# Performance work log

Hardware: AMD Instinct MI355X
Metric: run time of the kernel (lower is better)

Reference implementation:

```python
import jax, jax.numpy as jnp
import numpy as np

B, L, D, HD = 8, 4096, 1024, 16
H = D // HD


def setup_inputs() -> dict:
    key = jax.random.key(0)
    ks = jax.random.split(key, 16)
    s = 0.02
    return {
        "x": jax.random.normal(ks[0], (B, L, D), dtype=jnp.float32),
        "gamma": jnp.ones((D,), jnp.float32),
        "beta": jnp.zeros((D,), jnp.float32),
        "qw": jax.random.normal(ks[1], (D, D), jnp.float32) * s,
        "qb": jnp.zeros((D,), jnp.float32),
        "kw": jax.random.normal(ks[2], (D, D), jnp.float32) * s,
        "kb": jnp.zeros((D,), jnp.float32),
        "vw": jax.random.normal(ks[3], (D, D), jnp.float32) * s,
        "vb": jnp.zeros((D,), jnp.float32),
        "ow": jax.random.normal(ks[4], (D, D), jnp.float32) * s,
        "ob": jnp.zeros((D,), jnp.float32),
        "iw": jax.random.normal(ks[5], (H, D), jnp.float32) * s,
        "ib": jnp.zeros((H,), jnp.float32),
        "fw": jax.random.normal(ks[6], (H, D), jnp.float32) * s,
        "fb": jnp.zeros((H,), jnp.float32),
    }


def _layernorm(x, gamma, beta, eps=1e-5):
    mu = jnp.mean(x, axis=-1, keepdims=True)
    var = jnp.mean(jnp.square(x - mu), axis=-1, keepdims=True)
    return (x - mu) * jax.lax.rsqrt(var + eps) * gamma + beta


def _forward(x, gamma, beta, qw, qb, kw, kb, vw, vb, ow, ob, iw, ib, fw, fb):
    b, l, d = x.shape
    h_, dh = H, HD
    xn = _layernorm(x, gamma, beta)                    # [B,L,D]
    # Projections vectorized over time (the per-step norm/proj is time-independent)
    q = (xn @ qw.T + qb).reshape(b, l, h_, dh)
    k = ((xn @ kw.T + kb) / np.sqrt(dh)).reshape(b, l, h_, dh)
    v = (xn @ vw.T + vb).reshape(b, l, h_, dh)
    i_t = xn @ iw.T + ib                               # [B,L,H]
    f_t = xn @ fw.T + fb                               # [B,L,H]

    def step(carry, inp):
        C, n, m = carry
        qt, kt, vt, it, ft = inp                       # [B,H,Dh]x3, [B,H]x2
        m_new = jnp.maximum(ft + m, it)
        f = jnp.exp(ft + m - m_new)                    # [B,H]
        i = jnp.exp(it - m_new)                        # [B,H]
        vk = jnp.einsum('bhd,bhe->bhde', vt, kt)
        C_new = f[..., None, None] * C + i[..., None, None] * vk
        n_new = f[..., None] * n + i[..., None] * kt
        Cq = jnp.einsum('bhde,bhd->bhe', C_new, qt)
        denom = jnp.maximum(jnp.abs(jnp.sum(n_new * qt, axis=-1, keepdims=True)), 1.0)
        ht = (Cq / denom).reshape(b, d)
        return (C_new, n_new, m_new), ht

    init = (jnp.zeros((b, h_, dh, dh), x.dtype),
            jnp.zeros((b, h_, dh), x.dtype),
            jnp.zeros((b, h_), x.dtype))
    xs = (jnp.swapaxes(q, 0, 1), jnp.swapaxes(k, 0, 1), jnp.swapaxes(v, 0, 1),
          jnp.swapaxes(i_t, 0, 1), jnp.swapaxes(f_t, 0, 1))
    _, hs = jax.lax.scan(step, init, xs)               # [L,B,D]
    hs = jnp.swapaxes(hs, 0, 1)                        # [B,L,D]
    out = hs @ ow.T + ob
    return x + out                                     # dropout is identity in eval


def reference(x, gamma, beta, qw, qb, kw, kb, vw, vb, ow, ob, iw, ib, fw, fb):
    return _forward(x, gamma, beta, qw, qb, kw, kb, vw, vb, ow, ob, iw, ib, fw, fb)
```

## Files before the change

kernel.cpp:

```cpp
#include <hip/hip_runtime.h>
#include <stdint.h>

#define Bq 8
#define Lq 4096
#define Dq 1024
#define Hq 64
#define Mq (Bq*Lq)
#define CH 64
#define NC (Lq/CH)
#define TC (Bq*Hq*NC)
#define RECF 288

typedef short bf16x8 __attribute__((ext_vector_type(8)));
typedef float f32x4  __attribute__((ext_vector_type(4)));

__device__ __forceinline__ float b2f(unsigned short u) {
  union { unsigned int i; float f; } v; v.i = ((unsigned int)u) << 16; return v.f;
}
__device__ __forceinline__ unsigned short f2b(float f) {
  union { float f; unsigned int i; } v; v.f = f;
  unsigned int r = v.i + 0x7fffu + ((v.i >> 16) & 1u);
  return (unsigned short)(r >> 16);
}
__device__ __forceinline__ bf16x8 pack8(float4 a, float4 b) {
  bf16x8 r;
  r[0] = (short)f2b(a.x); r[1] = (short)f2b(a.y); r[2] = (short)f2b(a.z); r[3] = (short)f2b(a.w);
  r[4] = (short)f2b(b.x); r[5] = (short)f2b(b.y); r[6] = (short)f2b(b.z); r[7] = (short)f2b(b.w);
  return r;
}

__device__ __forceinline__ void gload_lds16(const unsigned short* g, unsigned short* l) {
  __builtin_amdgcn_global_load_lds(
      (const __attribute__((address_space(1))) unsigned int*)g,
      (__attribute__((address_space(3))) unsigned int*)l, 16, 0, 0);
}

__global__ void classify_kernel(const unsigned short* __restrict__ w, unsigned int* flag) {
  __shared__ unsigned int s_nz, s_ib;
  if (threadIdx.x == 0) { s_nz = 0; s_ib = 0; }
  __syncthreads();
  unsigned int nz = 0, ib = 0;
  for (int i = threadIdx.x; i < 8192; i += 256) {
    unsigned short u = w[2 * i];
    if (u) {
      nz++;
      unsigned int e = (u >> 7) & 0xFFu;
      if (e >= 0x31u && e <= 0x9Du) ib++;
    }
  }
  atomicAdd(&s_nz, nz); atomicAdd(&s_ib, ib);
  __syncthreads();
  if (threadIdx.x == 0) *flag = (s_nz > 0 && 4u * s_ib >= 3u * s_nz) ? 1u : 0u;
}

__global__ void sentinel_kernel(unsigned short* out, int n) {
  int i = blockIdx.x * 256 + threadIdx.x;
  if (i < n) out[i] = 0x447A;
}

__global__ void wconv_kernel(const void* __restrict__ wv, unsigned short* __restrict__ o,
                             const unsigned int* __restrict__ flagp) {
  const int isbf = (int)*flagp;
  const size_t i = ((size_t)blockIdx.x * 256 + threadIdx.x) * 8;
  if (isbf) {
    *(bf16x8*)(o + i) = *(const bf16x8*)((const unsigned short*)wv + i);
  } else {
    const float* wf = (const float*)wv;
    float4 a = *(const float4*)(wf + i);
    float4 b = *(const float4*)(wf + i + 4);
    *(bf16x8*)(o + i) = pack8(a, b);
  }
}

__global__ void ln_kernel(const void* __restrict__ xv,
                          const void* __restrict__ gv,
                          const void* __restrict__ bev,
                          unsigned short* __restrict__ xn,
                          const unsigned int* __restrict__ flagp) {
  const int isbf = (int)*flagp;
  const int row = blockIdx.x;
  const int t = threadIdx.x;
  const size_t base = (size_t)row * Dq;
  float v0, v1, v2, v3, g0, g1, g2, g3, e0, e1, e2, e3;
  if (isbf) {
    ushort4 u  = *(const ushort4*)((const unsigned short*)xv + base + t * 4);
    ushort4 g  = *(const ushort4*)((const unsigned short*)gv + t * 4);
    ushort4 be = *(const ushort4*)((const unsigned short*)bev + t * 4);
    v0 = b2f(u.x); v1 = b2f(u.y); v2 = b2f(u.z); v3 = b2f(u.w);
    g0 = b2f(g.x); g1 = b2f(g.y); g2 = b2f(g.z); g3 = b2f(g.w);
    e0 = b2f(be.x); e1 = b2f(be.y); e2 = b2f(be.z); e3 = b2f(be.w);
  } else {
    float4 u  = *(const float4*)((const float*)xv + base + t * 4);
    float4 g  = *(const float4*)((const float*)gv + t * 4);
    float4 be = *(const float4*)((const float*)bev + t * 4);
    v0 = u.x; v1 = u.y; v2 = u.z; v3 = u.w;
    g0 = g.x; g1 = g.y; g2 = g.z; g3 = g.w;
    e0 = be.x; e1 = be.y; e2 = be.z; e3 = be.w;
  }
  float s  = v0 + v1 + v2 + v3;
  float ss = v0*v0 + v1*v1 + v2*v2 + v3*v3;
#pragma unroll
  for (int off = 32; off >= 1; off >>= 1) {
    s  += __shfl_xor(s,  off, 64);
    ss += __shfl_xor(ss, off, 64);
  }
  __shared__ float sb[8];
  const int w = t >> 6, lane = t & 63;
  if (lane == 0) { sb[w] = s; sb[4 + w] = ss; }
  __syncthreads();
  s  = sb[0] + sb[1] + sb[2] + sb[3];
  ss = sb[4] + sb[5] + sb[6] + sb[7];
  const float mu   = s * (1.0f / Dq);
  const float var  = ss * (1.0f / Dq) - mu * mu;
  const float rstd = rsqrtf(var + 1e-5f);
  ushort4 o;
  o.x = f2b((v0 - mu) * rstd * g0 + e0);
  o.y = f2b((v1 - mu) * rstd * g1 + e1);
  o.z = f2b((v2 - mu) * rstd * g2 + e2);
  o.w = f2b((v3 - mu) * rstd * g3 + e3);
  *(ushort4*)(xn + base + t * 4) = o;
}

__device__ __forceinline__ void gemm_epilogue(
    f32x4 acc[4][4], int row0, int col0, int wm, int wn, int lane,
    const void* biasv, const void* residv, void* out,
    int N, float scale, int out_mode, int out_layout, int isbf) {
  const int colL = lane & 15;
  const int rq   = lane >> 4;
  const int wf32 = (out_mode == 1) || (out_mode == 2 && !isbf);
#pragma unroll
  for (int nt = 0; nt < 4; ++nt) {
    const int col = col0 + wn * 64 + nt * 16 + colL;
    if (col >= N) continue;
    const float bv = isbf ? b2f(((const unsigned short*)biasv)[col])
                          : ((const float*)biasv)[col];
#pragma unroll
    for (int mt = 0; mt < 4; ++mt) {
      const int rowb = row0 + wm * 64 + mt * 16 + rq * 4;
#pragma unroll
      for (int r = 0; r < 4; ++r) {
        const int row = rowb + r;
        size_t idx;
        if (out_layout == 1) {
          const int bb2 = row >> 12, t = row & 4095;
          idx = ((((size_t)bb2 * Hq + (col >> 4)) << 12) + t) * 16 + (col & 15);
        } else if (out_layout == 2) {
          const int bb2 = row >> 12, t = row & 4095;
          idx = (((size_t)bb2 * Hq + col) << 12) + t;
        } else {
          idx = (size_t)row * N + col;
        }
        float val = (acc[mt][nt][r] + bv) * scale;
        if (residv) {
          const size_t ridx = (size_t)row * N + col;
          val += isbf ? b2f(((const unsigned short*)residv)[ridx])
                      : ((const float*)residv)[ridx];
        }
        if (wf32) ((float*)out)[idx] = val;
        else ((unsigned short*)out)[idx] = f2b(val);
      }
    }
  }
}

__global__ void gemm_bt(const unsigned short* __restrict__ A,
                        const void* __restrict__ Wv,
                        const void* __restrict__ biasv,
                        const void* __restrict__ residv,
                        void* __restrict__ out,
                        int N, int K, float scale, int out_mode, int out_layout,
                        const unsigned int* __restrict__ flagp) {
  __shared__ unsigned short smA[128 * 32];
  __shared__ unsigned short smB[128 * 32];
  const int isbf = (int)*flagp;
  const int tid  = threadIdx.x;
  const int w    = tid >> 6;
  const int lane = tid & 63;
  const int wm   = w >> 1;
  const int wn   = w & 1;
  const int row0 = blockIdx.x * 128;
  const int col0 = blockIdx.y * 128;

  const int c0 = tid, c1 = tid + 256;
  const int ar0 = row0 + (c0 >> 2), ak0 = (c0 & 3) * 8;
  const int ar1 = row0 + (c1 >> 2), ak1 = (c1 & 3) * 8;
  int br0 = col0 + (c0 >> 2), bk0 = (c0 & 3) * 8;
  int br1 = col0 + (c1 >> 2), bk1 = (c1 & 3) * 8;
  if (br0 >= N) br0 = N - 1;
  if (br1 >= N) br1 = N - 1;
  const size_t aro0 = (size_t)ar0 * K + ak0;
  const size_t aro1 = (size_t)ar1 * K + ak1;
  const size_t bro0 = (size_t)br0 * K + bk0;
  const size_t bro1 = (size_t)br1 * K + bk1;

  f32x4 acc[4][4];
#pragma unroll
  for (int i = 0; i < 4; ++i)
#pragma unroll
    for (int j = 0; j < 4; ++j) acc[i][j] = (f32x4){0.f, 0.f, 0.f, 0.f};

  const int mrow = lane & 15;
  const int kq8  = (lane >> 4) * 8;

  for (int k0 = 0; k0 < K; k0 += 32) {
    bf16x8 ta0 = *(const bf16x8*)(A + aro0 + k0);
    bf16x8 ta1 = *(const bf16x8*)(A + aro1 + k0);
    bf16x8 tb0, tb1;
    if (isbf) {
      const unsigned short* W = (const unsigned short*)Wv;
      tb0 = *(const bf16x8*)(W + bro0 + k0);
      tb1 = *(const bf16x8*)(W + bro1 + k0);
    } else {
      const float* W = (const float*)Wv;
      float4 w00 = *(const float4*)(W + bro0 + k0);
      float4 w01 = *(const float4*)(W + bro0 + k0 + 4);
      float4 w10 = *(const float4*)(W + bro1 + k0);
      float4 w11 = *(const float4*)(W + bro1 + k0 + 4);
      tb0 = pack8(w00, w01);
      tb1 = pack8(w10, w11);
    }
    __syncthreads();
    *(bf16x8*)(smA + c0 * 8) = ta0;
    *(bf16x8*)(smA + c1 * 8) = ta1;
    *(bf16x8*)(smB + c0 * 8) = tb0;
    *(bf16x8*)(smB + c1 * 8) = tb1;
    __syncthreads();
    bf16x8 a[4], bb[4];
#pragma unroll
    for (int mt = 0; mt < 4; ++mt)
      a[mt] = *(const bf16x8*)(smA + (wm * 64 + mt * 16 + mrow) * 32 + kq8);
#pragma unroll
    for (int nt = 0; nt < 4; ++nt)
      bb[nt] = *(const bf16x8*)(smB + (wn * 64 + nt * 16 + mrow) * 32 + kq8);
#pragma unroll
    for (int mt = 0; mt < 4; ++mt)
#pragma unroll
      for (int nt = 0; nt < 4; ++nt)
        acc[mt][nt] = __builtin_amdgcn_mfma_f32_16x16x32_bf16(a[mt], bb[nt], acc[mt][nt], 0, 0, 0);
  }
  gemm_epilogue(acc, row0, col0, wm, wn, lane, biasv, residv, out,
                N, scale, out_mode, out_layout, isbf);
}

__global__ void __launch_bounds__(256)
gemm16(const unsigned short* __restrict__ A,
       const unsigned short* __restrict__ W,
       const void* __restrict__ biasv,
       const void* __restrict__ residv,
       void* __restrict__ out,
       float scale, int out_mode, int out_layout,
       const unsigned int* __restrict__ flagp) {
  __shared__ unsigned short smA[128 * 32];
  __shared__ unsigned short smB[128 * 32];
  const int isbf = (int)*flagp;
  const int tid  = threadIdx.x;
  const int w    = tid >> 6;
  const int lane = tid & 63;
  const int wm   = w >> 1;
  const int wn   = w & 1;
  const int row0 = blockIdx.x * 128;
  const int col0 = blockIdx.y * 128;

  const int rA0 = (w * 2) * 16 + (lane >> 2);
  const size_t aoff0 = (size_t)(row0 + rA0) * Dq + (lane & 3) * 8;
  const size_t aoff1 = aoff0 + (size_t)16 * Dq;
  const size_t boff0 = (size_t)(col0 + rA0) * Dq + (lane & 3) * 8;
  const size_t boff1 = boff0 + (size_t)16 * Dq;
  unsigned short* ldsA0 = smA + w * 1024;
  unsigned short* ldsA1 = smA + w * 1024 + 512;
  unsigned short* ldsB0 = smB + w * 1024;
  unsigned short* ldsB1 = smB + w * 1024 + 512;

  f32x4 acc[4][4];
#pragma unroll
  for (int i = 0; i < 4; ++i)
#pragma unroll
    for (int j = 0; j < 4; ++j) acc[i][j] = (f32x4){0.f, 0.f, 0.f, 0.f};

  const int mrow = lane & 15;
  const int kq8  = (lane >> 4) * 8;

  for (int k0 = 0; k0 < Dq; k0 += 32) {
    __syncthreads();
    gload_lds16(A + aoff0 + k0, ldsA0);
    gload_lds16(A + aoff1 + k0, ldsA1);
    gload_lds16(W + boff0 + k0, ldsB0);
    gload_lds16(W + boff1 + k0, ldsB1);
    __syncthreads();
    bf16x8 a[4], bb[4];
#pragma unroll
    for (int mt = 0; mt < 4; ++mt)
      a[mt] = *(const bf16x8*)(smA + (wm * 64 + mt * 16 + mrow) * 32 + kq8);
#pragma unroll
    for (int nt = 0; nt < 4; ++nt)
      bb[nt] = *(const bf16x8*)(smB + (wn * 64 + nt * 16 + mrow) * 32 + kq8);
#pragma unroll
    for (int mt = 0; mt < 4; ++mt)
#pragma unroll
      for (int nt = 0; nt < 4; ++nt)
        acc[mt][nt] = __builtin_amdgcn_mfma_f32_16x16x32_bf16(a[mt], bb[nt], acc[mt][nt], 0, 0, 0);
  }
  gemm_epilogue(acc, row0, col0, wm, wn, lane, biasv, residv, out,
                Dq, scale, out_mode, out_layout, isbf);
}

__device__ __forceinline__ void deposit16(float* __restrict__ dstrow, int xw,
                                          bf16x8 lo, bf16x8 hi) {
  float t[16];
#pragma unroll
  for (int j = 0; j < 8; ++j) t[j] = b2f((unsigned short)lo[j]);
#pragma unroll
  for (int j = 0; j < 8; ++j) t[8 + j] = b2f((unsigned short)hi[j]);
#pragma unroll
  for (int qd = 0; qd < 4; ++qd) {
    *(float4*)(dstrow + ((qd << 2) ^ xw)) =
        make_float4(t[qd * 4], t[qd * 4 + 1], t[qd * 4 + 2], t[qd * 4 + 3]);
  }
}


__global__ void __launch_bounds__(64, 1)
summary_kernel(const unsigned short* __restrict__ k,
               const unsigned short* __restrict__ v,
               const float* __restrict__ itg,
               const float* __restrict__ ftg,
               float* __restrict__ sum) {
  __shared__ float sk[CH * 16], sv[CH * 16], sp[CH];
  const int bid = blockIdx.x;
  const int bh  = bid >> 6;
  const int c   = bid & 63;
  const int lane = threadIdx.x;
  const int e  = lane & 15;
  const int dg = lane >> 4;
  const int d0 = dg * 4;
  const size_t qkvb = ((size_t)bh * Lq + (size_t)c * CH) * 16;
  const size_t gb   = (size_t)bh * Lq + (size_t)c * CH;

  float fv = ftg[gb + lane];
  float iv = itg[gb + lane];
  float F = fv;
#pragma unroll
  for (int off = 1; off < 64; off <<= 1) {
    float tt = __shfl_up(F, off, 64);
    if (lane >= off) F += tt;
  }
  float wv = iv - F;
  float Ml = wv;
#pragma unroll
  for (int off = 1; off < 64; off <<= 1)
    Ml = fmaxf(Ml, __shfl_xor(Ml, off, 64));
  const float Ftot = __shfl(F, 63, 64);

  const int xw = ((lane >> 1) & 3) << 2;
  {
    const unsigned short* kp = k + qkvb + (size_t)lane * 16;
    const unsigned short* vp = v + qkvb + (size_t)lane * 16;
    bf16x8 a0 = *(const bf16x8*)kp, a1 = *(const bf16x8*)(kp + 8);
    bf16x8 b0 = *(const bf16x8*)vp, b1 = *(const bf16x8*)(vp + 8);
    deposit16(sk + lane * 16, xw, a0, a1);
    deposit16(sv + lane * 16, xw, b0, b1);
    sp[lane] = __expf(wv - Ml);
  }
  float C0 = 0, C1 = 0, C2 = 0, C3 = 0;
  float g0 = 0, g1 = 0, g2 = 0, g3 = 0;
#pragma unroll 4
  for (int s = 0; s < CH; ++s) {
    const int x = ((s >> 1) & 3) << 2;
    const float* kr = sk + s * 16;
    const float* vr = sv + s * 16;
    const float p  = sp[s];
    const float ke = kr[e ^ x];
    const float4 kq = *(const float4*)(kr + (d0 ^ x));
    const float4 vq = *(const float4*)(vr + (d0 ^ x));
    const float a = p * ke;
    C0 = fmaf(a, vq.x, C0); C1 = fmaf(a, vq.y, C1);
    C2 = fmaf(a, vq.z, C2); C3 = fmaf(a, vq.w, C3);
    g0 = fmaf(p, kq.x, g0); g1 = fmaf(p, kq.y, g1);
    g2 = fmaf(p, kq.z, g2); g3 = fmaf(p, kq.w, g3);
  }
  float* rec = sum + (size_t)bid * RECF;
  *(float4*)(rec + e * 16 + d0) = make_float4(C0, C1, C2, C3);
  if (e == 0) *(float4*)(rec + 256 + d0) = make_float4(g0, g1, g2, g3);
  if (lane == 0) { rec[272] = Ml; rec[273] = Ftot; }
}

__global__ void __launch_bounds__(64, 1)
combine_kernel(float* __restrict__ sum) {
  const int bh = blockIdx.x;
  const int lane = threadIdx.x;
  float* base = sum + (size_t)bh * NC * RECF;
  float4 Sc = make_float4(0.f, 0.f, 0.f, 0.f);
  float Sn = 0.f;
  float m = 0.f;
  float4 G = *(float4*)(base + lane * 4);
  float gn = (lane < 16) ? base[256 + lane] : 0.f;
  float Ml = base[272], F = base[273];
  for (int c = 0; c < NC; ++c) {
    float* rec = base + (size_t)c * RECF;
    float4 Gn = make_float4(0.f, 0.f, 0.f, 0.f);
    float gnn = 0.f, Mln = 0.f, Fn = 0.f;
    if (c + 1 < NC) {
      float* rn = rec + RECF;
      Gn = *(float4*)(rn + lane * 4);
      if (lane < 16) gnn = rn[256 + lane];
      Mln = rn[272]; Fn = rn[273];
    }
    *(float4*)(rec + lane * 4) = Sc;
    if (lane < 16) rec[256 + lane] = Sn;
    if (lane == 0) rec[272] = m;
    const float mx = fmaxf(m, Ml);
    const float al = __expf(m - mx);
    const float be = __expf(Ml - mx);
    Sc.x = fmaf(al, Sc.x, be * G.x);
    Sc.y = fmaf(al, Sc.y, be * G.y);
    Sc.z = fmaf(al, Sc.z, be * G.z);
    Sc.w = fmaf(al, Sc.w, be * G.w);
    Sn = fmaf(al, Sn, be * gn);
    m = F + mx;
    G = Gn; gn = gnn; Ml = Mln; F = Fn;
  }
}

__global__ void __launch_bounds__(64, 1)
chunk_scan_kernel(const unsigned short* __restrict__ q,
                  const unsigned short* __restrict__ k,
                  const unsigned short* __restrict__ v,
                  const float* __restrict__ itg,
                  const float* __restrict__ ftg,
                  const float* __restrict__ sum,
                  unsigned short* __restrict__ hout) {
  __shared__ float sk[CH * 16], sq[CH * 16], sv[CH * 16], sg[2 * CH];
  const int bid = blockIdx.x;
  const int bh  = bid >> 6;
  const int c   = bid & 63;
  const int b   = bh >> 6;
  const int h   = bh & 63;
  const int lane = threadIdx.x;
  const int e  = lane & 15;
  const int dg = lane >> 4;
  const int d0 = dg * 4;
  const size_t qkvb = ((size_t)bh * Lq + (size_t)c * CH) * 16;
  const size_t gb   = (size_t)bh * Lq + (size_t)c * CH;
  const size_t ob   = (size_t)b * Lq * Dq + (size_t)h * 16 + (size_t)c * CH * Dq;

  const float* rec = sum + (size_t)bid * RECF;
  const float4 Cv = *(const float4*)(rec + e * 16 + d0);
  const float4 nv = *(const float4*)(rec + 256 + d0);
  float m = rec[272];
  float C0 = Cv.x, C1 = Cv.y, C2 = Cv.z, C3 = Cv.w;
  float n0 = nv.x, n1 = nv.y, n2 = nv.z, n3 = nv.w;

  const int xw = ((lane >> 1) & 3) << 2;
  {
    const unsigned short* kp = k + qkvb + (size_t)lane * 16;
    const unsigned short* qp = q + qkvb + (size_t)lane * 16;
    const unsigned short* vp = v + qkvb + (size_t)lane * 16;
    bf16x8 a0 = *(const bf16x8*)kp, a1 = *(const bf16x8*)(kp + 8);
    bf16x8 b0 = *(const bf16x8*)qp, b1 = *(const bf16x8*)(qp + 8);
    bf16x8 c0v = *(const bf16x8*)vp, c1v = *(const bf16x8*)(vp + 8);
    deposit16(sk + lane * 16, xw, a0, a1);
    deposit16(sq + lane * 16, xw, b0, b1);
    deposit16(sv + lane * 16, xw, c0v, c1v);
    sg[lane] = itg[gb + lane];
    sg[CH + lane] = ftg[gb + lane];
  }

#pragma unroll 4
  for (int s = 0; s < CH; ++s) {
    const int x = ((s >> 1) & 3) << 2;
    const float* kr = sk + s * 16;
    const float* qr = sq + s * 16;
    const float* vr = sv + s * 16;
    const float itc = sg[s];
    const float ftc = sg[CH + s];
    const float ke  = kr[e ^ x];
    const float4 kq4 = *(const float4*)(kr + (d0 ^ x));
    const float4 qq4 = *(const float4*)(qr + (d0 ^ x));
    const float4 vq4 = *(const float4*)(vr + (d0 ^ x));
    const float fm = ftc + m;
    const float mn = fmaxf(fm, itc);
    const float fg = __expf(fm - mn);
    const float ig = __expf(itc - mn);
    m = mn;
    const float a = ig * ke;
    C0 = fmaf(fg, C0, a * vq4.x);
    C1 = fmaf(fg, C1, a * vq4.y);
    C2 = fmaf(fg, C2, a * vq4.z);
    C3 = fmaf(fg, C3, a * vq4.w);
    n0 = fmaf(fg, n0, ig * kq4.x);
    n1 = fmaf(fg, n1, ig * kq4.y);
    n2 = fmaf(fg, n2, ig * kq4.z);
    n3 = fmaf(fg, n3, ig * kq4.w);
    float cq = fmaf(C3, qq4.w, fmaf(C2, qq4.z, fmaf(C1, qq4.y, C0 * qq4.x)));
    float dn = fmaf(n3, qq4.w, fmaf(n2, qq4.z, fmaf(n1, qq4.y, n0 * qq4.x)));
    cq += __shfl_xor(cq, 16, 64);
    cq += __shfl_xor(cq, 32, 64);
    dn += __shfl_xor(dn, 16, 64);
    dn += __shfl_xor(dn, 32, 64);
    const float denom = fmaxf(fabsf(dn), 1.0f);
    if (dg == 0) hout[ob + (size_t)s * Dq + e] = f2b(cq / denom);
  }
}

__global__ void __launch_bounds__(64, 1)
scan_kernel(const unsigned short* __restrict__ q,
            const unsigned short* __restrict__ k,
            const unsigned short* __restrict__ v,
            const float* __restrict__ itg,
            const float* __restrict__ ftg,
            unsigned short* __restrict__ hout) {
  __shared__ float sk[CH * 16], sq[CH * 16], sv[CH * 16], sg[2 * CH];
  const int bh = blockIdx.x;
  const int b  = bh >> 6;
  const int h  = bh & 63;
  const int lane = threadIdx.x;
  const int e  = lane & 15;
  const int dg = lane >> 4;
  const int d0 = dg * 4;
  const size_t qkvb = (size_t)bh * Lq * 16;
  const size_t gb   = (size_t)bh * Lq;
  const size_t ob   = (size_t)b * Lq * Dq + (size_t)h * 16;

  float C0 = 0, C1 = 0, C2 = 0, C3 = 0;
  float n0 = 0, n1 = 0, n2 = 0, n3 = 0;
  float m = 0.f;

  bf16x8 rk0, rk1, rq0, rq1, rv0, rv1;
  float rit, rft;
  {
    const unsigned short* kp = k + qkvb + (size_t)lane * 16;
    const unsigned short* qp = q + qkvb + (size_t)lane * 16;
    const unsigned short* vp = v + qkvb + (size_t)lane * 16;
    rk0 = *(const bf16x8*)kp; rk1 = *(const bf16x8*)(kp + 8);
    rq0 = *(const bf16x8*)qp; rq1 = *(const bf16x8*)(qp + 8);
    rv0 = *(const bf16x8*)vp; rv1 = *(const bf16x8*)(vp + 8);
    rit = itg[gb + lane]; rft = ftg[gb + lane];
  }

  const int xw = ((lane >> 1) & 3) << 2;
  const int NT = Lq / CH;
  for (int c = 0; c < NT; ++c) {
    deposit16(sk + lane * 16, xw, rk0, rk1);
    deposit16(sq + lane * 16, xw, rq0, rq1);
    deposit16(sv + lane * 16, xw, rv0, rv1);
    sg[lane] = rit; sg[CH + lane] = rft;
    if (c + 1 < NT) {
      const size_t off = qkvb + ((size_t)(c + 1) * CH + lane) * 16;
      const unsigned short* kp = k + off;
      const unsigned short* qp = q + off;
      const unsigned short* vp = v + off;
      rk0 = *(const bf16x8*)kp; rk1 = *(const bf16x8*)(kp + 8);
      rq0 = *(const bf16x8*)qp; rq1 = *(const bf16x8*)(qp + 8);
      rv0 = *(const bf16x8*)vp; rv1 = *(const bf16x8*)(vp + 8);
      rit = itg[gb + (size_t)(c + 1) * CH + lane];
      rft = ftg[gb + (size_t)(c + 1) * CH + lane];
    }
#pragma unroll 4
    for (int s = 0; s < CH; ++s) {
      const int x = ((s >> 1) & 3) << 2;
      const float* kr = sk + s * 16;
      const float* qr = sq + s * 16;
      const float* vr = sv + s * 16;
      const float itc = sg[s];
      const float ftc = sg[CH + s];
      const float ke  = kr[e ^ x];
      const float4 kq4 = *(const float4*)(kr + (d0 ^ x));
      const float4 qq4 = *(const float4*)(qr + (d0 ^ x));
      const float4 vq4 = *(const float4*)(vr + (d0 ^ x));
      const float fm = ftc + m;
      const float mn = fmaxf(fm, itc);
      const float fg = __expf(fm - mn);
      const float ig = __expf(itc - mn);
      m = mn;
      const float a = ig * ke;
      C0 = fmaf(fg, C0, a * vq4.x);
      C1 = fmaf(fg, C1, a * vq4.y);
      C2 = fmaf(fg, C2, a * vq4.z);
      C3 = fmaf(fg, C3, a * vq4.w);
      n0 = fmaf(fg, n0, ig * kq4.x);
      n1 = fmaf(fg, n1, ig * kq4.y);
      n2 = fmaf(fg, n2, ig * kq4.z);
      n3 = fmaf(fg, n3, ig * kq4.w);
      float cq = fmaf(C3, qq4.w, fmaf(C2, qq4.z, fmaf(C1, qq4.y, C0 * qq4.x)));
      float dn = fmaf(n3, qq4.w, fmaf(n2, qq4.z, fmaf(n1, qq4.y, n0 * qq4.x)));
      cq += __shfl_xor(cq, 16, 64);
      cq += __shfl_xor(cq, 32, 64);
      dn += __shfl_xor(dn, 16, 64);
      dn += __shfl_xor(dn, 32, 64);
      const float denom = fmaxf(fabsf(dn), 1.0f);
      if (dg == 0) hout[ob + (size_t)(c * CH + s) * Dq + e] = f2b(cq / denom);
    }
  }
}

extern "C" void kernel_launch(void* const* d_in, const int* in_sizes, int n_in,
                              void* d_out, int out_size, void* d_ws, size_t ws_size,
                              hipStream_t stream) {
  const void* x     = d_in[0];
  const void* gamma = d_in[1];
  const void* beta  = d_in[2];
  const void* qw    = d_in[3];
  const void* qbv   = d_in[4];
  const void* kw    = d_in[5];
  const void* kbv   = d_in[6];
  const void* vw    = d_in[7];
  const void* vbv   = d_in[8];
  const void* ow    = d_in[9];
  const void* obv   = d_in[10];
  const void* iw    = d_in[11];
  const void* ibv   = d_in[12];
  const void* fw    = d_in[13];
  const void* fbv   = d_in[14];

  const size_t bufBytes  = (size_t)Mq * Dq * 2;
  const size_t gateBytes = (size_t)Mq * Hq * 4;
  const size_t sumBytes  = (size_t)TC * RECF * 4;
  const size_t wBytes    = (size_t)Dq * Dq * 2;
  const size_t need_old   = 4 * bufBytes + 2 * gateBytes + 4096;
  const size_t need_chunk = need_old + sumBytes;
  const size_t need_fast  = need_chunk + 4 * wBytes;
  if (ws_size < need_old) {
    sentinel_kernel<<<(out_size + 255) / 256, 256, 0, stream>>>((unsigned short*)d_out, out_size);
    return;
  }
  const int chunked = (ws_size >= need_chunk);
  const int fast    = (ws_size >= need_fast);

  char* ws = (char*)d_ws;
  unsigned short* xnb = (unsigned short*)ws; ws += bufBytes;
  unsigned short* qbf = (unsigned short*)ws; ws += bufBytes;
  unsigned short* kbf = (unsigned short*)ws; ws += bufBytes;
  unsigned short* vbf = (unsigned short*)ws; ws += bufBytes;
  float* itb = (float*)ws; ws += gateBytes;
  float* ftb = (float*)ws; ws += gateBytes;
  unsigned int* flagp = (unsigned int*)ws; ws += 4096;
  float* sumb = (float*)ws; ws += sumBytes;
  unsigned short* wqb = (unsigned short*)ws; ws += wBytes;
  unsigned short* wkb = (unsigned short*)ws; ws += wBytes;
  unsigned short* wvb = (unsigned short*)ws; ws += wBytes;
  unsigned short* wob = (unsigned short*)ws; ws += wBytes;
  unsigned short* hbf = xnb;

  classify_kernel<<<1, 256, 0, stream>>>((const unsigned short*)qw, flagp);
  ln_kernel<<<Mq, 256, 0, stream>>>(x, gamma, beta, xnb, flagp);
  if (fast) {
    const int wgrid = (Dq * Dq / 8) / 256;
    wconv_kernel<<<wgrid, 256, 0, stream>>>(qw, wqb, flagp);
    wconv_kernel<<<wgrid, 256, 0, stream>>>(kw, wkb, flagp);
    wconv_kernel<<<wgrid, 256, 0, stream>>>(vw, wvb, flagp);
    wconv_kernel<<<wgrid, 256, 0, stream>>>(ow, wob, flagp);
    gemm16<<<dim3(Mq / 128, Dq / 128), 256, 0, stream>>>(xnb, wqb, qbv, nullptr, qbf, 1.0f,  0, 1, flagp);
    gemm16<<<dim3(Mq / 128, Dq / 128), 256, 0, stream>>>(xnb, wkb, kbv, nullptr, kbf, 0.25f, 0, 1, flagp);
    gemm16<<<dim3(Mq / 128, Dq / 128), 256, 0, stream>>>(xnb, wvb, vbv, nullptr, vbf, 1.0f,  0, 1, flagp);
  } else {
    gemm_bt<<<dim3(Mq / 128, 8), 256, 0, stream>>>(xnb, qw, qbv, nullptr, qbf, Dq, Dq, 1.0f,  0, 1, flagp);
    gemm_bt<<<dim3(Mq / 128, 8), 256, 0, stream>>>(xnb, kw, kbv, nullptr, kbf, Dq, Dq, 0.25f, 0, 1, flagp);
    gemm_bt<<<dim3(Mq / 128, 8), 256, 0, stream>>>(xnb, vw, vbv, nullptr, vbf, Dq, Dq, 1.0f,  0, 1, flagp);
  }
  gemm_bt<<<dim3(Mq / 128, 1), 256, 0, stream>>>(xnb, iw, ibv, nullptr, itb, Hq, Dq, 1.0f,  1, 2, flagp);
  gemm_bt<<<dim3(Mq / 128, 1), 256, 0, stream>>>(xnb, fw, fbv, nullptr, ftb, Hq, Dq, 1.0f,  1, 2, flagp);
  if (chunked) {
    summary_kernel<<<TC, 64, 0, stream>>>(kbf, vbf, itb, ftb, sumb);
    combine_kernel<<<Bq * Hq, 64, 0, stream>>>(sumb);
    chunk_scan_kernel<<<TC, 64, 0, stream>>>(qbf, kbf, vbf, itb, ftb, sumb, hbf);
  } else {
    scan_kernel<<<Bq * Hq, 64, 0, stream>>>(qbf, kbf, vbf, itb, ftb, hbf);
  }
  if (fast) {
    gemm16<<<dim3(Mq / 128, Dq / 128), 256, 0, stream>>>(hbf, wob, obv, x, d_out, 1.0f, 2, 0, flagp);
  } else {
    gemm_bt<<<dim3(Mq / 128, 8), 256, 0, stream>>>(hbf, ow, obv, x, d_out, Dq, Dq, 1.0f, 2, 0, flagp);
  }
}
```

Before: 1.215 ms.

## Remap GEMM tiles per XCD and compute chunk summaries with split-bf16 MFMA

The GEMM grid becomes one-dimensional, and block indices are remapped so that each of the 8 XCDs handles a contiguous band of 32 row tiles across all 8 column tiles. This is meant to improve L2 reuse of the A rows within each XCD. Separately, the chunk summary kernel now keeps k and v as bf16 in shared memory and computes the 16x16 C outer-product sum with MFMA 16x16x32 bf16 instructions. The p*v operand is split into hi and lo bf16 parts to preserve accuracy, which adds conversion work and a small precision risk in exchange for fewer scalar FMAs.

```diff
diff --git a/kernel.cpp b/kernel.cpp
--- a/kernel.cpp
+++ b/kernel.cpp
@@ -258,8 +258,13 @@
   const int lane = tid & 63;
   const int wm   = w >> 1;
   const int wn   = w & 1;
-  const int row0 = blockIdx.x * 128;
-  const int col0 = blockIdx.y * 128;
+  const int o    = blockIdx.x;
+  const int xcd  = o & 7;
+  const int slot = o >> 3;
+  const int rloc = slot >> 3;
+  const int cloc = slot & 7;
+  const int row0 = (xcd * 32 + rloc) * 128;
+  const int col0 = cloc * 128;
 
   const int rA0 = (w * 2) * 16 + (lane >> 2);
   const size_t aoff0 = (size_t)(row0 + rA0) * Dq + (lane & 3) * 8;
@@ -325,14 +330,13 @@
                const float* __restrict__ itg,
                const float* __restrict__ ftg,
                float* __restrict__ sum) {
-  __shared__ float sk[CH * 16], sv[CH * 16], sp[CH];
+  __shared__ unsigned short skb[CH * 16];
+  __shared__ unsigned short svb[CH * 16];
+  __shared__ float sp[CH];
   const int bid = blockIdx.x;
   const int bh  = bid >> 6;
   const int c   = bid & 63;
   const int lane = threadIdx.x;
-  const int e  = lane & 15;
-  const int dg = lane >> 4;
-  const int d0 = dg * 4;
   const size_t qkvb = ((size_t)bh * Lq + (size_t)c * CH) * 16;
   const size_t gb   = (size_t)bh * Lq + (size_t)c * CH;
 
@@ -351,36 +355,48 @@
     Ml = fmaxf(Ml, __shfl_xor(Ml, off, 64));
   const float Ftot = __shfl(F, 63, 64);
 
-  const int xw = ((lane >> 1) & 3) << 2;
   {
     const unsigned short* kp = k + qkvb + (size_t)lane * 16;
     const unsigned short* vp = v + qkvb + (size_t)lane * 16;
-    bf16x8 a0 = *(const bf16x8*)kp, a1 = *(const bf16x8*)(kp + 8);
-    bf16x8 b0 = *(const bf16x8*)vp, b1 = *(const bf16x8*)(vp + 8);
-    deposit16(sk + lane * 16, xw, a0, a1);
-    deposit16(sv + lane * 16, xw, b0, b1);
+    *(bf16x8*)(skb + lane * 16)     = *(const bf16x8*)kp;
+    *(bf16x8*)(skb + lane * 16 + 8) = *(const bf16x8*)(kp + 8);
+    *(bf16x8*)(svb + lane * 16)     = *(const bf16x8*)vp;
+    *(bf16x8*)(svb + lane * 16 + 8) = *(const bf16x8*)(vp + 8);
     sp[lane] = __expf(wv - Ml);
   }
-  float C0 = 0, C1 = 0, C2 = 0, C3 = 0;
-  float g0 = 0, g1 = 0, g2 = 0, g3 = 0;
-#pragma unroll 4
-  for (int s = 0; s < CH; ++s) {
-    const int x = ((s >> 1) & 3) << 2;
-    const float* kr = sk + s * 16;
-    const float* vr = sv + s * 16;
-    const float p  = sp[s];
-    const float ke = kr[e ^ x];
-    const float4 kq = *(const float4*)(kr + (d0 ^ x));
-    const float4 vq = *(const float4*)(vr + (d0 ^ x));
-    const float a = p * ke;
-    C0 = fmaf(a, vq.x, C0); C1 = fmaf(a, vq.y, C1);
-    C2 = fmaf(a, vq.z, C2); C3 = fmaf(a, vq.w, C3);
-    g0 = fmaf(p, kq.x, g0); g1 = fmaf(p, kq.y, g1);
-    g2 = fmaf(p, kq.z, g2); g3 = fmaf(p, kq.w, g3);
-  }
+
+  const int e  = lane & 15;
+  const int sg = lane >> 4;
+
+  float nacc = 0.f;
+#pragma unroll
+  for (int j = 0; j < 16; ++j) {
+    const int s = sg * 16 + j;
+    nacc = fmaf(sp[s], b2f(skb[s * 16 + e]), nacc);
+  }
+  nacc += __shfl_xor(nacc, 16, 64);
+  nacc += __shfl_xor(nacc, 32, 64);
+
+  f32x4 acc = (f32x4){0.f, 0.f, 0.f, 0.f};
+#pragma unroll
+  for (int kk = 0; kk < 2; ++kk) {
+    bf16x8 ahi, alo, bfr;
+#pragma unroll
+    for (int j = 0; j < 8; ++j) {
+      const int s = kk * 32 + sg * 8 + j;
+      const float pv = sp[s] * b2f(svb[s * 16 + e]);
+      const unsigned short hi = f2b(pv);
+      ahi[j] = (short)hi;
+      alo[j] = (short)f2b(pv - b2f(hi));
+      bfr[j] = (short)skb[s * 16 + e];
+    }
+    acc = __builtin_amdgcn_mfma_f32_16x16x32_bf16(ahi, bfr, acc, 0, 0, 0);
+    acc = __builtin_amdgcn_mfma_f32_16x16x32_bf16(alo, bfr, acc, 0, 0, 0);
+  }
+
   float* rec = sum + (size_t)bid * RECF;
-  *(float4*)(rec + e * 16 + d0) = make_float4(C0, C1, C2, C3);
-  if (e == 0) *(float4*)(rec + 256 + d0) = make_float4(g0, g1, g2, g3);
+  *(f32x4*)(rec + e * 16 + sg * 4) = acc;
+  if (sg == 0) rec[256 + e] = nacc;
   if (lane == 0) { rec[272] = Ml; rec[273] = Ftot; }
 }
 
@@ -649,9 +665,9 @@
     wconv_kernel<<<wgrid, 256, 0, stream>>>(kw, wkb, flagp);
     wconv_kernel<<<wgrid, 256, 0, stream>>>(vw, wvb, flagp);
     wconv_kernel<<<wgrid, 256, 0, stream>>>(ow, wob, flagp);
-    gemm16<<<dim3(Mq / 128, Dq / 128), 256, 0, stream>>>(xnb, wqb, qbv, nullptr, qbf, 1.0f,  0, 1, flagp);
-    gemm16<<<dim3(Mq / 128, Dq / 128), 256, 0, stream>>>(xnb, wkb, kbv, nullptr, kbf, 0.25f, 0, 1, flagp);
-    gemm16<<<dim3(Mq / 128, Dq / 128), 256, 0, stream>>>(xnb, wvb, vbv, nullptr, vbf, 1.0f,  0, 1, flagp);
+    gemm16<<<dim3(2048), 256, 0, stream>>>(xnb, wqb, qbv, nullptr, qbf, 1.0f,  0, 1, flagp);
+    gemm16<<<dim3(2048), 256, 0, stream>>>(xnb, wkb, kbv, nullptr, kbf, 0.25f, 0, 1, flagp);
+    gemm16<<<dim3(2048), 256, 0, stream>>>(xnb, wvb, vbv, nullptr, vbf, 1.0f,  0, 1, flagp);
   } else {
     gemm_bt<<<dim3(Mq / 128, 8), 256, 0, stream>>>(xnb, qw, qbv, nullptr, qbf, Dq, Dq, 1.0f,  0, 1, flagp);
     gemm_bt<<<dim3(Mq / 128, 8), 256, 0, stream>>>(xnb, kw, kbv, nullptr, kbf, Dq, Dq, 0.25f, 0, 1, flagp);
@@ -667,7 +683,7 @@
     scan_kernel<<<Bq * Hq, 64, 0, stream>>>(qbf, kbf, vbf, itb, ftb, hbf);
   }
   if (fast) {
-    gemm16<<<dim3(Mq / 128, Dq / 128), 256, 0, stream>>>(hbf, wob, obv, x, d_out, 1.0f, 2, 0, flagp);
+    gemm16<<<dim3(2048), 256, 0, stream>>>(hbf, wob, obv, x, d_out, 1.0f, 2, 0, flagp);
   } else {
     gemm_bt<<<dim3(Mq / 128, 8), 256, 0, stream>>>(hbf, ow, obv, x, d_out, Dq, Dq, 1.0f, 2, 0, flagp);
   }
```

New measurement: 1.161 ms. -4.4%, faster.
